# Performance work log

Hardware: AMD Instinct MI355X
Metric: run time of the kernel (lower is better)

## Reference

```python
import jax, jax.numpy as jnp
import numpy as np

G = 256           # graphs in batch
NPG = 360         # nodes per graph (hard-coded in_nodes)
N = G * NPG       # 92160 total nodes
DEG = 16          # average degree
E = N * DEG       # 1474560 edges
H = 5             # first_layer_heads
C = 30            # hidden_dim
IN = 11           # in_channels
NUM_GC = 9        # number of GraphConv layers after EGAT
EPS = 1e-5


def setup_inputs() -> dict:
    key = jax.random.key(0)
    ks = jax.random.split(key, 16)
    x = jax.random.normal(ks[0], (N, IN), jnp.float32)
    # intra-graph random edges (graph-major node ordering)
    src = jax.random.randint(ks[1], (E,), 0, NPG)
    dst = jax.random.randint(ks[2], (E,), 0, NPG)
    off = jnp.repeat(jnp.arange(G, dtype=jnp.int32) * NPG, NPG * DEG)
    edge_index = jnp.stack([src + off, dst + off]).astype(jnp.int32)
    edge_attr = jax.random.uniform(ks[3], (E, 1), jnp.float32)
    batch_mask = jnp.repeat(jnp.arange(G, dtype=jnp.int32), NPG)
    s = 0.1
    egat_w = jax.random.normal(ks[4], (IN, H, C), jnp.float32) * s
    att_src = jax.random.normal(ks[5], (H, C), jnp.float32) * s
    att_dst = jax.random.normal(ks[6], (H, C), jnp.float32) * s
    att_edge = jax.random.normal(ks[7], (1, H), jnp.float32) * s
    gc_w_root = jax.random.normal(ks[8], (NUM_GC, C, C), jnp.float32) * s
    gc_w_nbr = jax.random.normal(ks[9], (NUM_GC, C, C), jnp.float32) * s
    gc_b = jnp.zeros((NUM_GC, C), jnp.float32)
    fc1_w = jax.random.normal(ks[10], (10 * C, 50), jnp.float32) * s
    fc1_b = jnp.zeros((50,), jnp.float32)
    fc2_w = jax.random.normal(ks[11], (50, 2), jnp.float32) * s
    fc2_b = jnp.zeros((2,), jnp.float32)
    return dict(x=x, edge_index=edge_index, edge_attr=edge_attr, batch_mask=batch_mask,
                egat_w=egat_w, att_src=att_src, att_dst=att_dst, att_edge=att_edge,
                gc_w_root=gc_w_root, gc_w_nbr=gc_w_nbr, gc_b=gc_b,
                fc1_w=fc1_w, fc1_b=fc1_b, fc2_w=fc2_w, fc2_b=fc2_b)


def _instance_norm(h, seg):
    # per-graph, per-feature normalization (PyG InstanceNorm, affine=False)
    cnt = jax.ops.segment_sum(jnp.ones((h.shape[0], 1), h.dtype), seg, G)
    mean = jax.ops.segment_sum(h, seg, G) / cnt
    var = jax.ops.segment_sum(h * h, seg, G) / cnt - mean * mean
    return (h - mean[seg]) * jax.lax.rsqrt(var[seg] + EPS)


def reference(x, edge_index, edge_attr, batch_mask,
              egat_w, att_src, att_dst, att_edge,
              gc_w_root, gc_w_nbr, gc_b, fc1_w, fc1_b, fc2_w, fc2_b):
    src, dst = edge_index[0], edge_index[1]
    # ---- EGATConv (heads=5, concat=False -> mean over heads) ----
    xp = jnp.einsum('ni,ihc->nhc', x, egat_w)                    # [N,H,C]
    logit = ((xp[src] * att_src).sum(-1) + (xp[dst] * att_dst).sum(-1)
             + edge_attr @ att_edge)                              # [E,H]
    logit = jax.nn.leaky_relu(logit, 0.2)
    m = jax.ops.segment_max(logit, dst, N)                        # [N,H]
    m = jnp.where(jnp.isfinite(m), m, 0.0)
    ex = jnp.exp(logit - m[dst])
    denom = jax.ops.segment_sum(ex, dst, N)
    alpha = ex / (denom[dst] + 1e-16)                             # [E,H]
    h = jax.ops.segment_sum(alpha[:, :, None] * xp[src], dst, N).mean(axis=1)  # [N,C]
    ew = alpha.mean(-1)                                           # new edge_attr, viewed(-1)
    h = _instance_norm(h, batch_mask)
    outs = [h]
    for l in range(NUM_GC):
        msg = jax.ops.segment_sum(ew[:, None] * (h @ gc_w_nbr[l])[src], dst, N)
        h = h @ gc_w_root[l] + msg + gc_b[l]
        h = _instance_norm(h, batch_mask)
        outs.append(h)
    # ---- per-graph max pooling over nodes, concat all block outputs ----
    pooled = jnp.concatenate([o.reshape(G, NPG, -1).max(axis=1) for o in outs], axis=-1)  # [G,300]
    fc_out = jax.nn.relu(pooled @ fc1_w + fc1_b) @ fc2_w + fc2_b  # [G,2]
    return fc_out
```

## Files before the change

### kernel.cpp

```cpp
#include <hip/hip_runtime.h>
#include <hip/hip_fp16.h>

#define GN 256
#define NPG 360
#define NN (GN*NPG)
#define DEGAVG 16
#define EE (NN*DEGAVG)
#define EPG (NPG*DEGAVG)
#define HH 5
#define CC 30
#define IN_CH 11
#define NUM_GC 9
#define EPS 1e-5f

#define HLS 35
#define AGS 33
#define SSS 5
#define XS 12

#define OFF_HL     0
#define OFF_EDGE   50400
#define OFF_UNI    73440
#define OFF_ROWP   120960
#define OFF_DEG    121688
#define OFF_POOL   123128
#define OFF_FCH    124328
#define OFF_WA     124552
#define OFF_WSUM   125000
#define SMEM_TOTAL 125072

__device__ __forceinline__ float f16_to_f32(unsigned short us) {
  __half_raw r; r.x = us; return __half2float(r);
}
__device__ __forceinline__ unsigned short f32_to_f16(float f) {
  __half h = __float2half(f);
  __half_raw r = *reinterpret_cast<__half_raw*>(&h);
  return r.x;
}

__device__ __forceinline__ void norm_pool(float* h_l, float* pooled_l, int layer, int tid) {
  int c = tid >> 5, jj = tid & 31;
  if (c < CC) {
    float va[12];
    float s = 0.f, s2 = 0.f;
#pragma unroll
    for (int t = 0; t < 12; t++) {
      int i = jj + t * 32;
      float v = (i < NPG) ? h_l[i * HLS + c] : 0.f;
      va[t] = v; s += v; s2 += v * v;
    }
#pragma unroll
    for (int m = 16; m >= 1; m >>= 1) { s += __shfl_xor(s, m); s2 += __shfl_xor(s2, m); }
    float mean = s * (1.f / NPG);
    float rs = rsqrtf(s2 * (1.f / NPG) - mean * mean + EPS);
    float mx = -1e30f;
#pragma unroll
    for (int t = 0; t < 12; t++) {
      int i = jj + t * 32;
      if (i < NPG) {
        float v = (va[t] - mean) * rs;
        h_l[i * HLS + c] = v;
        mx = fmaxf(mx, v);
      }
    }
#pragma unroll
    for (int m = 16; m >= 1; m >>= 1) mx = fmaxf(mx, __shfl_xor(mx, m));
    if (jj == 0) pooled_l[layer * CC + c] = mx;
  }
}

template <int CB>
__device__ __forceinline__ void mm_half(int n, const float* h_l, const float* agg_l,
                                        const float* Wr, const float* Wn, const float* bs,
                                        float* acc) {
#pragma unroll
  for (int c = 0; c < 15; c++) acc[c] = bs[CB + c];
  const float* hr = h_l + n * HLS;
  const float* ar = agg_l + n * AGS;
#pragma unroll
  for (int k = 0; k < CC; k++) {
    float hk = hr[k];
#pragma unroll
    for (int c = 0; c < 15; c++) acc[c] = fmaf(hk, Wr[k * CC + CB + c], acc[c]);
  }
#pragma unroll
  for (int k = 0; k < CC; k++) {
    float ak = ar[k];
#pragma unroll
    for (int c = 0; c < 15; c++) acc[c] = fmaf(ak, Wn[k * CC + CB + c], acc[c]);
  }
}

__global__ __launch_bounds__(1024, 4) void k_mega(
    const float* __restrict__ x, const int* __restrict__ ei, const float* __restrict__ eattr,
    const float* __restrict__ egw, const float* __restrict__ att_s,
    const float* __restrict__ att_d, const float* __restrict__ att_e,
    const float* __restrict__ wroot, const float* __restrict__ wnbr,
    const float* __restrict__ gcb,
    const float* __restrict__ fc1w, const float* __restrict__ fc1b,
    const float* __restrict__ fc2w, const float* __restrict__ fc2b,
    float* __restrict__ out) {
  __shared__ __align__(16) unsigned char smem[SMEM_TOTAL];
  float*          h_l     = (float*)(smem + OFF_HL);
  unsigned*       edge_l  = (unsigned*)(smem + OFF_EDGE);
  float*          x_l     = (float*)(smem + OFF_UNI);
  float*          ssrc_l  = (float*)(smem + OFF_UNI) + NPG * XS;
  float*          sdst_l  = (float*)(smem + OFF_UNI) + NPG * XS + NPG * SSS;
  float*          agg_l   = (float*)(smem + OFF_UNI);
  unsigned short* rowp_l  = (unsigned short*)(smem + OFF_ROWP);
  unsigned*       deg_l   = (unsigned*)(smem + OFF_DEG);
  float*          pooled_l= (float*)(smem + OFF_POOL);
  float*          fch     = (float*)(smem + OFF_FCH);
  float*          wa_l    = (float*)(smem + OFF_WA);
  unsigned*       wsum    = (unsigned*)(smem + OFF_WSUM);

  const int g = blockIdx.x, tid = threadIdx.x;
  const int nb = g * NPG;
  const int ebase = g * EPG;
  const int lane = tid & 63, wid = tid >> 6;

  for (int i = tid; i < NPG; i += 1024) deg_l[i] = 0u;
  for (int it = tid; it < NPG * XS; it += 1024) {
    int n = it / XS, i = it - n * XS;
    x_l[it] = (i < IN_CH) ? x[(size_t)(nb + n) * IN_CH + i] : 0.f;
  }
  __syncthreads();

  for (int e = tid; e < EPG; e += 1024) {
    int d = ei[EE + ebase + e] - nb;
    atomicAdd(&deg_l[d], 1u);
  }
  if (tid < 110) {
    int half = tid >= 55;
    int idx = tid - half * 55;
    int i = idx / 5, h = idx - i * 5;
    const float* av = half ? att_d : att_s;
    float s = 0.f;
#pragma unroll
    for (int c = 0; c < CC; c++) s += egw[(i * HH + h) * CC + c] * av[h * CC + c];
    wa_l[tid] = s;
  }
  __syncthreads();

  {
    unsigned v = (tid < NPG) ? deg_l[tid] : 0u;
#pragma unroll
    for (int off = 1; off < 64; off <<= 1) {
      unsigned t = (unsigned)__shfl_up((int)v, off);
      if (lane >= off) v += t;
    }
    if (lane == 63) wsum[wid] = v;
    __syncthreads();
    if (tid == 0) {
      unsigned run = 0;
      for (int i = 0; i < 16; i++) { unsigned t = wsum[i]; wsum[i] = run; run += t; }
    }
    __syncthreads();
    if (tid < NPG) rowp_l[tid + 1] = (unsigned short)(v + wsum[wid]);
    if (tid == 0) rowp_l[0] = 0;
    if (tid < NPG) deg_l[tid] = 0u;
  }
  __syncthreads();

  for (int e = tid; e < EPG; e += 1024) {
    int s = ei[ebase + e] - nb;
    int d = ei[EE + ebase + e] - nb;
    float ea = eattr[ebase + e];
    unsigned pos = (unsigned)rowp_l[d] + atomicAdd(&deg_l[d], 1u);
    edge_l[pos] = (unsigned)s | ((unsigned)f32_to_f16(ea) << 16);
  }
  if (tid < NPG) {
    float xi[IN_CH];
#pragma unroll
    for (int i = 0; i < IN_CH; i++) xi[i] = x_l[tid * XS + i];
#pragma unroll
    for (int h = 0; h < HH; h++) {
      float s1 = 0.f, s2 = 0.f;
#pragma unroll
      for (int i = 0; i < IN_CH; i++) {
        s1 = fmaf(xi[i], wa_l[i * HH + h], s1);
        s2 = fmaf(xi[i], wa_l[55 + i * HH + h], s2);
      }
      ssrc_l[tid * SSS + h] = s1;
      sdst_l[tid * SSS + h] = s2;
    }
  }
  __syncthreads();

  if (tid < NPG) {
    const int n = tid;
    const int b = rowp_l[n], en = rowp_l[n + 1];
    float sd[HH], ae[HH];
#pragma unroll
    for (int h = 0; h < HH; h++) { sd[h] = sdst_l[n * SSS + h]; ae[h] = att_e[h]; }
    float dn[HH];
#pragma unroll
    for (int h = 0; h < HH; h++) dn[h] = 0.f;
    int p = b;
    for (; p + 1 < en; p += 2) {
      unsigned ua = edge_l[p], ub = edge_l[p + 1];
      int sa_ = ua & 0xffffu, sb_ = ub & 0xffffu;
      float eaa = f16_to_f32((unsigned short)(ua >> 16));
      float eab = f16_to_f32((unsigned short)(ub >> 16));
      const float* sra = ssrc_l + sa_ * SSS;
      const float* srb = ssrc_l + sb_ * SSS;
#pragma unroll
      for (int h = 0; h < HH; h++) {
        float la = sra[h] + sd[h] + eaa * ae[h];
        float lb = srb[h] + sd[h] + eab * ae[h];
        la = la > 0.f ? la : 0.2f * la;
        lb = lb > 0.f ? lb : 0.2f * lb;
        dn[h] += __expf(la) + __expf(lb);
      }
    }
    if (p < en) {
      unsigned u = edge_l[p];
      int s = u & 0xffffu;
      float ea = f16_to_f32((unsigned short)(u >> 16));
      const float* sr = ssrc_l + s * SSS;
#pragma unroll
      for (int h = 0; h < HH; h++) {
        float lg = sr[h] + sd[h] + ea * ae[h];
        lg = lg > 0.f ? lg : 0.2f * lg;
        dn[h] += __expf(lg);
      }
    }
    float rdn[HH];
#pragma unroll
    for (int h = 0; h < HH; h++) rdn[h] = 1.f / (dn[h] + 1e-16f);
    float gg[55];
#pragma unroll
    for (int k = 0; k < 55; k++) gg[k] = 0.f;
    for (p = b; p < en; p++) {
      unsigned u = edge_l[p];
      int s = u & 0xffffu;
      float ea = f16_to_f32((unsigned short)(u >> 16));
      const float* sr = ssrc_l + s * SSS;
      const float* xr = x_l + s * XS;
      const float4 xv0 = *(const float4*)(xr);
      const float4 xv1 = *(const float4*)(xr + 4);
      const float4 xv2 = *(const float4*)(xr + 8);
      const float xi[IN_CH] = {xv0.x, xv0.y, xv0.z, xv0.w, xv1.x, xv1.y, xv1.z, xv1.w,
                               xv2.x, xv2.y, xv2.z};
      float ews = 0.f;
#pragma unroll
      for (int h = 0; h < HH; h++) {
        float lg = sr[h] + sd[h] + ea * ae[h];
        lg = lg > 0.f ? lg : 0.2f * lg;
        float a = __expf(lg) * rdn[h];
        ews += a;
#pragma unroll
        for (int i = 0; i < IN_CH; i++) gg[h * IN_CH + i] = fmaf(a, xi[i], gg[h * IN_CH + i]);
      }
      edge_l[p] = (unsigned)(s * HLS) | ((unsigned)f32_to_f16(ews * 0.2f) << 16);
    }
#pragma unroll
    for (int half = 0; half < 2; half++) {
      float acc[15];
#pragma unroll
      for (int c = 0; c < 15; c++) acc[c] = 0.f;
#pragma unroll
      for (int i = 0; i < IN_CH; i++) {
#pragma unroll
        for (int h = 0; h < HH; h++) {
          float gv = gg[h * IN_CH + i];
          const float* wr = egw + (i * HH + h) * CC + half * 15;
#pragma unroll
          for (int c = 0; c < 15; c++) acc[c] = fmaf(gv, wr[c], acc[c]);
        }
      }
#pragma unroll
      for (int c = 0; c < 15; c++) h_l[n * HLS + half * 15 + c] = 0.2f * acc[c];
    }
  }
  __syncthreads();

  norm_pool(h_l, pooled_l, 0, tid);
  __syncthreads();

  const int es = lane >> 5;
  const int cg = lane & 31;
#pragma unroll 1
  for (int l = 0; l < NUM_GC; l++) {
    for (int n = wid; n < NPG; n += 16) {
      int b = rowp_l[n], en = rowp_l[n + 1];
      float a0 = 0.f, a1 = 0.f, a2 = 0.f, a3 = 0.f;
      int p = b + es;
      for (; p + 6 < en; p += 8) {
        unsigned u0 = edge_l[p];
        unsigned u1 = edge_l[p + 2];
        unsigned u2 = edge_l[p + 4];
        unsigned u3 = edge_l[p + 6];
        float h0 = h_l[(u0 & 0xffffu) + cg];
        float h1 = h_l[(u1 & 0xffffu) + cg];
        float h2 = h_l[(u2 & 0xffffu) + cg];
        float h3 = h_l[(u3 & 0xffffu) + cg];
        a0 = fmaf(f16_to_f32((unsigned short)(u0 >> 16)), h0, a0);
        a1 = fmaf(f16_to_f32((unsigned short)(u1 >> 16)), h1, a1);
        a2 = fmaf(f16_to_f32((unsigned short)(u2 >> 16)), h2, a2);
        a3 = fmaf(f16_to_f32((unsigned short)(u3 >> 16)), h3, a3);
      }
      for (; p < en; p += 2) {
        unsigned u = edge_l[p];
        a0 = fmaf(f16_to_f32((unsigned short)(u >> 16)), h_l[(u & 0xffffu) + cg], a0);
      }
      float a = (a0 + a1) + (a2 + a3);
      a += __shfl_xor(a, 32);
      if (lane < CC) agg_l[n * AGS + lane] = a;
    }
    __syncthreads();
    const float* Wr = wroot + l * CC * CC;
    const float* Wn = wnbr + l * CC * CC;
    const float* bs = gcb + l * CC;
    float acc[15];
    int n = -1, cb = 0;
    if (tid < NPG) { n = tid; cb = 0; mm_half<0>(n, h_l, agg_l, Wr, Wn, bs, acc); }
    else if (tid >= 512 && tid < 512 + NPG) { n = tid - 512; cb = 15; mm_half<15>(n, h_l, agg_l, Wr, Wn, bs, acc); }
    __syncthreads();
    if (n >= 0) {
#pragma unroll
      for (int c = 0; c < 15; c++) h_l[n * HLS + cb + c] = acc[c];
    }
    __syncthreads();
    norm_pool(h_l, pooled_l, l + 1, tid);
    __syncthreads();
  }

  if (tid < 50) {
    float a = fc1b[tid];
    for (int i = 0; i < 10 * CC; i++) a = fmaf(pooled_l[i], fc1w[i * 50 + tid], a);
    fch[tid] = fmaxf(a, 0.f);
  }
  __syncthreads();
  if (tid < 2) {
    float o = fc2b[tid];
#pragma unroll
    for (int j = 0; j < 50; j++) o = fmaf(fch[j], fc2w[j * 2 + tid], o);
    out[g * 2 + tid] = o;
  }
}

extern "C" void kernel_launch(void* const* d_in, const int* in_sizes, int n_in,
                              void* d_out, int out_size, void* d_ws, size_t ws_size,
                              hipStream_t stream) {
  (void)d_ws; (void)ws_size; (void)in_sizes; (void)n_in; (void)out_size;
  const float* x     = (const float*)d_in[0];
  const int*   ei    = (const int*)d_in[1];
  const float* eattr = (const float*)d_in[2];
  const float* egw   = (const float*)d_in[4];
  const float* att_s = (const float*)d_in[5];
  const float* att_d = (const float*)d_in[6];
  const float* att_e = (const float*)d_in[7];
  const float* wroot = (const float*)d_in[8];
  const float* wnbr  = (const float*)d_in[9];
  const float* gcb   = (const float*)d_in[10];
  const float* fc1w  = (const float*)d_in[11];
  const float* fc1b  = (const float*)d_in[12];
  const float* fc2w  = (const float*)d_in[13];
  const float* fc2b  = (const float*)d_in[14];
  float* out = (float*)d_out;

  k_mega<<<GN, 1024, 0, stream>>>(x, ei, eattr, egw, att_s, att_d, att_e,
                                  wroot, wnbr, gcb, fc1w, fc1b, fc2w, fc2b, out);
}
```

Measured before the change: 219.6 us.

## Overlap root matmul with neighbor aggregation via warp specialization

Splits the block's 16 waves into roles. Waves 0-9 perform the edge gather/aggregation, while waves 10-15 (one thread per node, all 30 output channels) compute the root-weight matmul at the same time. After a barrier the same threads add the neighbor-weight matmul and write h in place, which removes one barrier and the separate writeback phase. Edge indices are also pre-scaled to byte offsets so the gather skips an address multiply. In exchange, aggregation runs on fewer waves, and each matmul thread now holds 30 accumulators, which raises register pressure.

```diff
diff --git a/kernel.cpp b/kernel.cpp
--- a/kernel.cpp
+++ b/kernel.cpp
@@ -66,28 +66,6 @@
 #pragma unroll
     for (int m = 16; m >= 1; m >>= 1) mx = fmaxf(mx, __shfl_xor(mx, m));
     if (jj == 0) pooled_l[layer * CC + c] = mx;
-  }
-}
-
-template <int CB>
-__device__ __forceinline__ void mm_half(int n, const float* h_l, const float* agg_l,
-                                        const float* Wr, const float* Wn, const float* bs,
-                                        float* acc) {
-#pragma unroll
-  for (int c = 0; c < 15; c++) acc[c] = bs[CB + c];
-  const float* hr = h_l + n * HLS;
-  const float* ar = agg_l + n * AGS;
-#pragma unroll
-  for (int k = 0; k < CC; k++) {
-    float hk = hr[k];
-#pragma unroll
-    for (int c = 0; c < 15; c++) acc[c] = fmaf(hk, Wr[k * CC + CB + c], acc[c]);
-  }
-#pragma unroll
-  for (int k = 0; k < CC; k++) {
-    float ak = ar[k];
-#pragma unroll
-    for (int c = 0; c < 15; c++) acc[c] = fmaf(ak, Wn[k * CC + CB + c], acc[c]);
   }
 }
 
@@ -252,7 +230,7 @@
 #pragma unroll
         for (int i = 0; i < IN_CH; i++) gg[h * IN_CH + i] = fmaf(a, xi[i], gg[h * IN_CH + i]);
       }
-      edge_l[p] = (unsigned)(s * HLS) | ((unsigned)f32_to_f16(ews * 0.2f) << 16);
+      edge_l[p] = (unsigned)(s * (HLS * 4)) | ((unsigned)f32_to_f16(ews * 0.2f) << 16);
     }
 #pragma unroll
     for (int half = 0; half < 2; half++) {
@@ -279,47 +257,67 @@
   __syncthreads();
 
   const int es = lane >> 5;
-  const int cg = lane & 31;
+  const int cg4 = (lane & 31) << 2;
+  const char* hb = (const char*)h_l;
+  const int nmm = tid - 640;
+  const bool mmact = (wid >= 10) && (nmm < NPG);
 #pragma unroll 1
   for (int l = 0; l < NUM_GC; l++) {
-    for (int n = wid; n < NPG; n += 16) {
-      int b = rowp_l[n], en = rowp_l[n + 1];
-      float a0 = 0.f, a1 = 0.f, a2 = 0.f, a3 = 0.f;
-      int p = b + es;
-      for (; p + 6 < en; p += 8) {
-        unsigned u0 = edge_l[p];
-        unsigned u1 = edge_l[p + 2];
-        unsigned u2 = edge_l[p + 4];
-        unsigned u3 = edge_l[p + 6];
-        float h0 = h_l[(u0 & 0xffffu) + cg];
-        float h1 = h_l[(u1 & 0xffffu) + cg];
-        float h2 = h_l[(u2 & 0xffffu) + cg];
-        float h3 = h_l[(u3 & 0xffffu) + cg];
-        a0 = fmaf(f16_to_f32((unsigned short)(u0 >> 16)), h0, a0);
-        a1 = fmaf(f16_to_f32((unsigned short)(u1 >> 16)), h1, a1);
-        a2 = fmaf(f16_to_f32((unsigned short)(u2 >> 16)), h2, a2);
-        a3 = fmaf(f16_to_f32((unsigned short)(u3 >> 16)), h3, a3);
-      }
-      for (; p < en; p += 2) {
-        unsigned u = edge_l[p];
-        a0 = fmaf(f16_to_f32((unsigned short)(u >> 16)), h_l[(u & 0xffffu) + cg], a0);
-      }
-      float a = (a0 + a1) + (a2 + a3);
-      a += __shfl_xor(a, 32);
-      if (lane < CC) agg_l[n * AGS + lane] = a;
-    }
-    __syncthreads();
     const float* Wr = wroot + l * CC * CC;
     const float* Wn = wnbr + l * CC * CC;
     const float* bs = gcb + l * CC;
-    float acc[15];
-    int n = -1, cb = 0;
-    if (tid < NPG) { n = tid; cb = 0; mm_half<0>(n, h_l, agg_l, Wr, Wn, bs, acc); }
-    else if (tid >= 512 && tid < 512 + NPG) { n = tid - 512; cb = 15; mm_half<15>(n, h_l, agg_l, Wr, Wn, bs, acc); }
-    __syncthreads();
-    if (n >= 0) {
-#pragma unroll
-      for (int c = 0; c < 15; c++) h_l[n * HLS + cb + c] = acc[c];
+    float acc[CC];
+    if (wid < 10) {
+      for (int n = wid; n < NPG; n += 10) {
+        int b = rowp_l[n], en = rowp_l[n + 1];
+        float a0 = 0.f, a1 = 0.f, a2 = 0.f, a3 = 0.f;
+        int p = b + es;
+        for (; p + 6 < en; p += 8) {
+          unsigned u0 = edge_l[p];
+          unsigned u1 = edge_l[p + 2];
+          unsigned u2 = edge_l[p + 4];
+          unsigned u3 = edge_l[p + 6];
+          float h0 = *(const float*)(hb + (u0 & 0xffffu) + cg4);
+          float h1 = *(const float*)(hb + (u1 & 0xffffu) + cg4);
+          float h2 = *(const float*)(hb + (u2 & 0xffffu) + cg4);
+          float h3 = *(const float*)(hb + (u3 & 0xffffu) + cg4);
+          a0 = fmaf(f16_to_f32((unsigned short)(u0 >> 16)), h0, a0);
+          a1 = fmaf(f16_to_f32((unsigned short)(u1 >> 16)), h1, a1);
+          a2 = fmaf(f16_to_f32((unsigned short)(u2 >> 16)), h2, a2);
+          a3 = fmaf(f16_to_f32((unsigned short)(u3 >> 16)), h3, a3);
+        }
+        for (; p < en; p += 2) {
+          unsigned u = edge_l[p];
+          a0 = fmaf(f16_to_f32((unsigned short)(u >> 16)),
+                    *(const float*)(hb + (u & 0xffffu) + cg4), a0);
+        }
+        float a = (a0 + a1) + (a2 + a3);
+        a += __shfl_xor(a, 32);
+        if ((lane & 31) < CC && es == 0) agg_l[n * AGS + (lane & 31)] = a;
+      }
+    } else if (mmact) {
+#pragma unroll
+      for (int c = 0; c < CC; c++) acc[c] = bs[c];
+      const float* hr = h_l + nmm * HLS;
+#pragma unroll
+      for (int k = 0; k < CC; k++) {
+        float hk = hr[k];
+#pragma unroll
+        for (int c = 0; c < CC; c++) acc[c] = fmaf(hk, Wr[k * CC + c], acc[c]);
+      }
+    }
+    __syncthreads();
+    if (mmact) {
+      const float* ar = agg_l + nmm * AGS;
+#pragma unroll
+      for (int k = 0; k < CC; k++) {
+        float ak = ar[k];
+#pragma unroll
+        for (int c = 0; c < CC; c++) acc[c] = fmaf(ak, Wn[k * CC + c], acc[c]);
+      }
+      float* ho = h_l + nmm * HLS;
+#pragma unroll
+      for (int c = 0; c < CC; c++) ho[c] = acc[c];
     }
     __syncthreads();
     norm_pool(h_l, pooled_l, l + 1, tid);
```

New measurement: 257.0 us. 17.0% more time.
